# Optimization experiments

Measured on AMD Instinct MI355X. Metric: run time of the kernel, lower is better.

## Reference

```python
import jax, jax.numpy as jnp
import numpy as np

N = 8192
F_IN = 256
F_OUT = 128
SLOPE = 0.2
NEG_INF = -9000000000000000.0


def setup_inputs() -> dict:
    key = jax.random.key(0)
    k1, k2, k3, k4, k5 = jax.random.split(key, 5)
    x = jax.random.normal(k1, (N, F_IN), dtype=jnp.float32)
    adj = jax.random.randint(k2, (N, N), 0, 2).astype(jnp.float32)
    W = jax.random.normal(k3, (F_IN, F_OUT), dtype=jnp.float32) * (1.0 / np.sqrt(F_IN))
    a_src = jax.random.normal(k4, (F_OUT,), dtype=jnp.float32) * (1.0 / np.sqrt(F_OUT))
    a_dst = jax.random.normal(k5, (F_OUT,), dtype=jnp.float32) * (1.0 / np.sqrt(F_OUT))
    return {"x": x, "adj": adj, "W": W, "a_src": a_src, "a_dst": a_dst}


def reference(x, adj, W, a_src, a_dst):
    # h: (N, F_OUT)
    h = x @ W
    f_src = h @ a_src  # (N,)
    f_dst = h @ a_dst  # (N,)
    # additive attention scores: (N, N)
    e = f_src[:, None] + f_dst[None, :]
    e = jnp.where(e >= 0, e, SLOPE * e)  # leaky_relu
    e = jnp.where(adj > 0, e, NEG_INF)
    alpha = jax.nn.softmax(e, axis=1)  # (N, N)
    return alpha @ h  # (N, F_OUT)
```

## Files before the change

### kernel.cpp

```cpp
#include <hip/hip_runtime.h>
#include <hip/hip_bf16.h>

#define NN 8192
#define FIN 256
#define FO 128
#define BROWS 16
#define NCH 32
#define L2E 1.4426950408889634f
#define C2  0.28853900817779268f

typedef __bf16 bf16x8 __attribute__((ext_vector_type(8)));
typedef __bf16 bf16x2 __attribute__((ext_vector_type(2)));
typedef float  f32x4  __attribute__((ext_vector_type(4)));
typedef unsigned long long u64;
typedef u64 u64x2 __attribute__((ext_vector_type(2)));

__device__ __forceinline__ f32x4 ntload(const float* p) {
  return __builtin_nontemporal_load((const f32x4*)p);
}

__global__ __launch_bounds__(256) void k_proj(
    const float* __restrict__ x, const float* __restrict__ W,
    const float* __restrict__ a_src, const float* __restrict__ a_dst,
    __bf16* __restrict__ Bp, float* __restrict__ f_src, float* __restrict__ f_dst)
{
  __shared__ float xs[16 * FIN];
  __shared__ float fs[16], fd[16];
  const int tid = threadIdx.x;
  const int i0 = blockIdx.x * 16;

  const float4* xg = (const float4*)(x + (size_t)i0 * FIN);
  float4* xs4 = (float4*)xs;
  #pragma unroll
  for (int t = 0; t < 4; t++) xs4[tid + 256 * t] = xg[tid + 256 * t];
  if (tid < 16) { fs[tid] = 0.f; fd[tid] = 0.f; }
  __syncthreads();

  const int cq = tid & 31;
  const int rg = tid >> 5;
  const int c0 = cq * 4;
  const int r0 = rg * 2;
  float acc0[4] = {0.f,0.f,0.f,0.f};
  float acc1[4] = {0.f,0.f,0.f,0.f};
  const float* xr0 = xs + r0 * FIN;
  const float* xr1 = xs + (r0 + 1) * FIN;

  for (int k = 0; k < FIN; k += 4) {
    float4 xa = *(const float4*)(xr0 + k);
    float4 xb = *(const float4*)(xr1 + k);
    #pragma unroll
    for (int kk = 0; kk < 4; kk++) {
      float4 wv = *(const float4*)(W + (size_t)(k + kk) * FO + c0);
      float xav = ((const float*)&xa)[kk];
      float xbv = ((const float*)&xb)[kk];
      acc0[0] += xav * wv.x; acc0[1] += xav * wv.y;
      acc0[2] += xav * wv.z; acc0[3] += xav * wv.w;
      acc1[0] += xbv * wv.x; acc1[1] += xbv * wv.y;
      acc1[2] += xbv * wv.z; acc1[3] += xbv * wv.w;
    }
  }

  float4 as = *(const float4*)(a_src + c0);
  float4 ad = *(const float4*)(a_dst + c0);
  float ps0 = acc0[0]*as.x + acc0[1]*as.y + acc0[2]*as.z + acc0[3]*as.w;
  float ps1 = acc1[0]*as.x + acc1[1]*as.y + acc1[2]*as.z + acc1[3]*as.w;
  float pd0 = acc0[0]*ad.x + acc0[1]*ad.y + acc0[2]*ad.z + acc0[3]*ad.w;
  float pd1 = acc1[0]*ad.x + acc1[1]*ad.y + acc1[2]*ad.z + acc1[3]*ad.w;
  atomicAdd(&fs[r0],     ps0);
  atomicAdd(&fs[r0 + 1], ps1);
  atomicAdd(&fd[r0],     pd0);
  atomicAdd(&fd[r0 + 1], pd1);

  const int j0 = i0 + r0;
  const int kg = j0 >> 5;
  const int q  = (j0 >> 3) & 3;
  const int t0 = j0 & 7;
  #pragma unroll
  for (int c = 0; c < 4; c++) {
    const int n = c0 + c;
    bf16x2 v;
    v[0] = (__bf16)acc0[c];
    v[1] = (__bf16)acc1[c];
    size_t idx = ((size_t)(kg * 8 + (n >> 4)) * 64 + q * 16 + (n & 15)) * 8 + t0;
    *(bf16x2*)(Bp + idx) = v;
  }
  __syncthreads();
  if (tid < 16) { f_src[i0 + tid] = fs[tid]; f_dst[i0 + tid] = fd[tid]; }
}

__global__ __launch_bounds__(512, 4) void k_attn(
    const float* __restrict__ adj, const __bf16* __restrict__ Bp,
    const float* __restrict__ f_src, const float* __restrict__ f_dst,
    float* __restrict__ out)
{
  __shared__ __align__(16) float G1s[2][256];
  __shared__ __align__(16) float G2s[2][256];
  __shared__ __align__(16) u64 msk[BROWS][6];
  __shared__ __align__(16) __bf16 af[8][64][8];
  __shared__ float lsum[BROWS];

  const int tid = threadIdx.x;
  const int w = tid >> 6;
  const int lane = tid & 63;
  const int m = lane & 15;
  const int q = lane >> 4;
  const int i0 = blockIdx.x * BROWS;

  const int sqA = w >> 1, kgA = w & 1;
  const int nq8 = w;
  const int tbl = tid >> 8, gcol = tid & 255;

  const float* abase = adj + (size_t)(i0 + 2 * w) * NN + lane * 4;
  f32x4 sA0 = ntload(abase);
  f32x4 sA1 = ntload(abase + NN);
  f32x4 sB0 = ntload(abase + 256);
  f32x4 sB1 = ntload(abase + NN + 256);

  {
    float d0 = f_dst[gcol];
    if (tbl == 0) G1s[0][gcol] = __builtin_amdgcn_exp2f(d0 * L2E);
    else          G2s[0][gcol] = __builtin_amdgcn_exp2f(d0 * C2);
  }
  float fdv = f_dst[256 + gcol];
  if (tid < BROWS) lsum[tid] = 0.f;
  float s = f_src[i0 + m];
  const float F1 = __builtin_amdgcn_exp2f(s * L2E);
  const float F2 = __builtin_amdgcn_exp2f(s * C2);

  f32x4 acc = (f32x4){0.f, 0.f, 0.f, 0.f};
  float psum = 0.f;

#define ITER(c, s0, s1)                                                       \
  {                                                                           \
            \
    u64 b0 = __ballot(s0[0] > 0.f), b1 = __ballot(s0[1] > 0.f);               \
    u64 b2 = __ballot(s0[2] > 0.f), b3 = __ballot(s0[3] > 0.f);               \
    if (lane < 4) msk[2*w][lane]   = lane==0?b0:lane==1?b1:lane==2?b2:b3;     \
    b0 = __ballot(s1[0] > 0.f); b1 = __ballot(s1[1] > 0.f);                   \
    b2 = __ballot(s1[2] > 0.f); b3 = __ballot(s1[3] > 0.f);                   \
    if (lane < 4) msk[2*w+1][lane] = lane==0?b0:lane==1?b1:lane==2?b2:b3;     \
    if ((c) + 1 < NCH) {                                                      \
      if (tbl == 0) G1s[((c)+1)&1][gcol] = __builtin_amdgcn_exp2f(fdv * L2E); \
      else          G2s[((c)+1)&1][gcol] = __builtin_amdgcn_exp2f(fdv * C2);  \
    }                                                                         \
    __syncthreads();                         \
                \
    {                                                                         \
      u64x2 Ma = *(const u64x2*)&msk[m][0];                                   \
      u64x2 Mb = *(const u64x2*)&msk[m][2];                                   \
      const u64 M0 = Ma[0], M1 = Ma[1], M2 = Mb[0], M3 = Mb[1];               \
      const int jl = sqA * 64 + kgA * 32 + q * 8;                             \
      float4 u0 = *(const float4*)(&G1s[(c)&1][jl]);                          \
      float4 u1 = *(const float4*)(&G1s[(c)&1][jl + 4]);                      \
      float4 v0 = *(const float4*)(&G2s[(c)&1][jl]);                          \
      float4 v1 = *(const float4*)(&G2s[(c)&1][jl + 4]);                      \
      const unsigned b = sqA * 16 + kgA * 8 + q * 2;                          \
      const unsigned e0 = (unsigned)(M0 >> b);                                \
      const unsigned e1 = (unsigned)(M1 >> b);                                \
      const unsigned e2 = (unsigned)(M2 >> b);                                \
      const unsigned e3 = (unsigned)(M3 >> b);                                \
      float p0 = (e0 & 1u) ? fmaxf(F1 * u0.x, F2 * v0.x) : 0.f;               \
      float p1 = (e1 & 1u) ? fmaxf(F1 * u0.y, F2 * v0.y) : 0.f;               \
      float p2 = (e2 & 1u) ? fmaxf(F1 * u0.z, F2 * v0.z) : 0.f;               \
      float p3 = (e3 & 1u) ? fmaxf(F1 * u0.w, F2 * v0.w) : 0.f;               \
      float p4 = (e0 & 2u) ? fmaxf(F1 * u1.x, F2 * v1.x) : 0.f;               \
      float p5 = (e1 & 2u) ? fmaxf(F1 * u1.y, F2 * v1.y) : 0.f;               \
      float p6 = (e2 & 2u) ? fmaxf(F1 * u1.z, F2 * v1.z) : 0.f;               \
      float p7 = (e3 & 2u) ? fmaxf(F1 * u1.w, F2 * v1.w) : 0.f;               \
      psum += ((p0 + p1) + (p2 + p3)) + ((p4 + p5) + (p6 + p7));              \
      bf16x8 a;                                                               \
      a[0] = (__bf16)p0; a[1] = (__bf16)p1; a[2] = (__bf16)p2;                \
      a[3] = (__bf16)p3; a[4] = (__bf16)p4; a[5] = (__bf16)p5;                \
      a[6] = (__bf16)p6; a[7] = (__bf16)p7;                                   \
      *(bf16x8*)&af[w][lane][0] = a;                                          \
    }                                                                         \
    __syncthreads();                                   \
                    \
    {                                                                         \
      const __bf16* bch = Bp + (size_t)(c) * 8 * 4096                         \
                          + (size_t)nq8 * 512 + lane * 8;                     \
      bf16x8 bf0 = *(const bf16x8*)(bch);                                     \
      bf16x8 bf1 = *(const bf16x8*)(bch + 4096);                              \
      bf16x8 bf2 = *(const bf16x8*)(bch + 2 * 4096);                          \
      bf16x8 bf3 = *(const bf16x8*)(bch + 3 * 4096);                          \
      bf16x8 bf4 = *(const bf16x8*)(bch + 4 * 4096);                          \
      bf16x8 bf5 = *(const bf16x8*)(bch + 5 * 4096);                          \
      bf16x8 bf6 = *(const bf16x8*)(bch + 6 * 4096);                          \
      bf16x8 bf7 = *(const bf16x8*)(bch + 7 * 4096);                          \
      bf16x8 a0 = *(const bf16x8*)&af[0][lane][0];                            \
      bf16x8 a1 = *(const bf16x8*)&af[1][lane][0];                            \
      bf16x8 a2 = *(const bf16x8*)&af[2][lane][0];                            \
      bf16x8 a3 = *(const bf16x8*)&af[3][lane][0];                            \
      bf16x8 a4 = *(const bf16x8*)&af[4][lane][0];                            \
      bf16x8 a5 = *(const bf16x8*)&af[5][lane][0];                            \
      bf16x8 a6 = *(const bf16x8*)&af[6][lane][0];                            \
      bf16x8 a7 = *(const bf16x8*)&af[7][lane][0];                            \
      acc = __builtin_amdgcn_mfma_f32_16x16x32_bf16(a0, bf0, acc, 0, 0, 0);   \
      acc = __builtin_amdgcn_mfma_f32_16x16x32_bf16(a1, bf1, acc, 0, 0, 0);   \
      acc = __builtin_amdgcn_mfma_f32_16x16x32_bf16(a2, bf2, acc, 0, 0, 0);   \
      acc = __builtin_amdgcn_mfma_f32_16x16x32_bf16(a3, bf3, acc, 0, 0, 0);   \
      acc = __builtin_amdgcn_mfma_f32_16x16x32_bf16(a4, bf4, acc, 0, 0, 0);   \
      acc = __builtin_amdgcn_mfma_f32_16x16x32_bf16(a5, bf5, acc, 0, 0, 0);   \
      acc = __builtin_amdgcn_mfma_f32_16x16x32_bf16(a6, bf6, acc, 0, 0, 0);   \
      acc = __builtin_amdgcn_mfma_f32_16x16x32_bf16(a7, bf7, acc, 0, 0, 0);   \
    }                                                                         \
     \
    if ((c) + 2 < NCH) {                                                      \
      s0 = ntload(abase + ((c) + 2) * 256);                                   \
      s1 = ntload(abase + NN + ((c) + 2) * 256);                              \
      fdv = f_dst[((c) + 2) * 256 + gcol];                                    \
    }                                                                         \
  }

  for (int c = 0; c < NCH; c += 2) {
    ITER(c, sA0, sA1)
    ITER(c + 1, sB0, sB1)
  }
#undef ITER

  {
    float p = psum;
    p += __shfl_xor(p, 16);
    p += __shfl_xor(p, 32);
    if (lane < 16) atomicAdd(&lsum[lane], p);
  }
  __syncthreads();

  #pragma unroll
  for (int r = 0; r < 4; ++r) {
    const int rr = q * 4 + r;
    const float inv = 1.0f / lsum[rr];
    out[(size_t)(i0 + rr) * FO + nq8 * 16 + m] = acc[r] * inv;
  }
}

extern "C" void kernel_launch(void* const* d_in, const int* in_sizes, int n_in,
                              void* d_out, int out_size, void* d_ws, size_t ws_size,
                              hipStream_t stream) {
  const float* x     = (const float*)d_in[0];
  const float* adj   = (const float*)d_in[1];
  const float* W     = (const float*)d_in[2];
  const float* a_src = (const float*)d_in[3];
  const float* a_dst = (const float*)d_in[4];
  float* out = (float*)d_out;

  char* ws = (char*)d_ws;
  __bf16* Bp   = (__bf16*)ws;
  float* f_src = (float*)(ws + 2097152);
  float* f_dst = (float*)(ws + 2097152 + 32768);

  hipLaunchKernelGGL(k_proj, dim3(512), dim3(256), 0, stream,
                     x, W, a_src, a_dst, Bp, f_src, f_dst);
  hipLaunchKernelGGL(k_attn, dim3(512), dim3(512), 0, stream,
                     adj, Bp, f_src, f_dst, out);
}
```

Before: 406.6 us.

## Double the attention chunk width to halve barrier rounds and deepen prefetch

The column chunk processed per iteration grows from 256 to 512, so each step builds masks for twice the columns, fills 16 bf16 A-fragments, and issues 16 MFMAs between barriers. This halves the number of __syncthreads rounds, and each prefetch now keeps eight adj vectors in flight. Scheduling barriers pin the prefetch loads after the MFMA block. In exchange it uses more registers and shared memory, which could reduce occupancy under the 512x4 launch bound.

```diff
diff --git a/kernel.cpp b/kernel.cpp
--- a/kernel.cpp
+++ b/kernel.cpp
@@ -5,7 +5,8 @@
 #define FIN 256
 #define FO 128
 #define BROWS 16
-#define NCH 32
+#define CC 512
+#define NCH 16
 #define L2E 1.4426950408889634f
 #define C2  0.28853900817779268f
 
@@ -93,10 +94,10 @@
     const float* __restrict__ f_src, const float* __restrict__ f_dst,
     float* __restrict__ out)
 {
-  __shared__ __align__(16) float G1s[2][256];
-  __shared__ __align__(16) float G2s[2][256];
-  __shared__ __align__(16) u64 msk[BROWS][6];
-  __shared__ __align__(16) __bf16 af[8][64][8];
+  __shared__ __align__(16) float G1s[2][CC];
+  __shared__ __align__(16) float G2s[2][CC];
+  __shared__ __align__(16) u64 msk[BROWS][10];
+  __shared__ __align__(16) __bf16 af[16][64][8];
   __shared__ float lsum[BROWS];
 
   const int tid = threadIdx.x;
@@ -106,22 +107,33 @@
   const int q = lane >> 4;
   const int i0 = blockIdx.x * BROWS;
 
-  const int sqA = w >> 1, kgA = w & 1;
   const int nq8 = w;
   const int tbl = tid >> 8, gcol = tid & 255;
 
+  float fdvA = f_dst[CC + gcol];
+  float fdvB = f_dst[CC + 256 + gcol];
+  __builtin_amdgcn_sched_barrier(0);
   const float* abase = adj + (size_t)(i0 + 2 * w) * NN + lane * 4;
-  f32x4 sA0 = ntload(abase);
-  f32x4 sA1 = ntload(abase + NN);
-  f32x4 sB0 = ntload(abase + 256);
-  f32x4 sB1 = ntload(abase + NN + 256);
+  f32x4 sA0a = ntload(abase);
+  f32x4 sA0b = ntload(abase + 256);
+  f32x4 sA1a = ntload(abase + NN);
+  f32x4 sA1b = ntload(abase + NN + 256);
+  f32x4 sB0a = ntload(abase + CC);
+  f32x4 sB0b = ntload(abase + CC + 256);
+  f32x4 sB1a = ntload(abase + NN + CC);
+  f32x4 sB1b = ntload(abase + NN + CC + 256);
 
   {
     float d0 = f_dst[gcol];
-    if (tbl == 0) G1s[0][gcol] = __builtin_amdgcn_exp2f(d0 * L2E);
-    else          G2s[0][gcol] = __builtin_amdgcn_exp2f(d0 * C2);
-  }
-  float fdv = f_dst[256 + gcol];
+    float d1 = f_dst[256 + gcol];
+    if (tbl == 0) {
+      G1s[0][gcol]       = __builtin_amdgcn_exp2f(d0 * L2E);
+      G1s[0][256 + gcol] = __builtin_amdgcn_exp2f(d1 * L2E);
+    } else {
+      G2s[0][gcol]       = __builtin_amdgcn_exp2f(d0 * C2);
+      G2s[0][256 + gcol] = __builtin_amdgcn_exp2f(d1 * C2);
+    }
+  }
   if (tid < BROWS) lsum[tid] = 0.f;
   float s = f_src[i0 + m];
   const float F1 = __builtin_amdgcn_exp2f(s * L2E);
@@ -129,32 +141,50 @@
 
   f32x4 acc = (f32x4){0.f, 0.f, 0.f, 0.f};
   float psum = 0.f;
-
-#define ITER(c, s0, s1)                                                       \
+  __syncthreads();
+
+#define ITER(c, s0a, s0b, s1a, s1b)                                           \
   {                                                                           \
-            \
-    u64 b0 = __ballot(s0[0] > 0.f), b1 = __ballot(s0[1] > 0.f);               \
-    u64 b2 = __ballot(s0[2] > 0.f), b3 = __ballot(s0[3] > 0.f);               \
-    if (lane < 4) msk[2*w][lane]   = lane==0?b0:lane==1?b1:lane==2?b2:b3;     \
-    b0 = __ballot(s1[0] > 0.f); b1 = __ballot(s1[1] > 0.f);                   \
-    b2 = __ballot(s1[2] > 0.f); b3 = __ballot(s1[3] > 0.f);                   \
-    if (lane < 4) msk[2*w+1][lane] = lane==0?b0:lane==1?b1:lane==2?b2:b3;     \
+              \
+    {                                                                         \
+      u64 b0 = __ballot(s0a[0] > 0.f), b1 = __ballot(s0a[1] > 0.f);           \
+      u64 b2 = __ballot(s0a[2] > 0.f), b3 = __ballot(s0a[3] > 0.f);           \
+      u64 b4 = __ballot(s0b[0] > 0.f), b5 = __ballot(s0b[1] > 0.f);           \
+      u64 b6 = __ballot(s0b[2] > 0.f), b7 = __ballot(s0b[3] > 0.f);           \
+      if (lane < 8)                                                           \
+        msk[2*w][lane] = lane==0?b0:lane==1?b1:lane==2?b2:lane==3?b3:         \
+                         lane==4?b4:lane==5?b5:lane==6?b6:b7;                 \
+      b0 = __ballot(s1a[0] > 0.f); b1 = __ballot(s1a[1] > 0.f);               \
+      b2 = __ballot(s1a[2] > 0.f); b3 = __ballot(s1a[3] > 0.f);               \
+      b4 = __ballot(s1b[0] > 0.f); b5 = __ballot(s1b[1] > 0.f);               \
+      b6 = __ballot(s1b[2] > 0.f); b7 = __ballot(s1b[3] > 0.f);               \
+      if (lane < 8)                                                           \
+        msk[2*w+1][lane] = lane==0?b0:lane==1?b1:lane==2?b2:lane==3?b3:       \
+                           lane==4?b4:lane==5?b5:lane==6?b6:b7;               \
+    }                                                                         \
     if ((c) + 1 < NCH) {                                                      \
-      if (tbl == 0) G1s[((c)+1)&1][gcol] = __builtin_amdgcn_exp2f(fdv * L2E); \
-      else          G2s[((c)+1)&1][gcol] = __builtin_amdgcn_exp2f(fdv * C2);  \
+      if (tbl == 0) {                                                         \
+        G1s[((c)+1)&1][gcol]       = __builtin_amdgcn_exp2f(fdvA * L2E);      \
+        G1s[((c)+1)&1][256 + gcol] = __builtin_amdgcn_exp2f(fdvB * L2E);      \
+      } else {                                                                \
+        G2s[((c)+1)&1][gcol]       = __builtin_amdgcn_exp2f(fdvA * C2);       \
+        G2s[((c)+1)&1][256 + gcol] = __builtin_amdgcn_exp2f(fdvB * C2);       \
+      }                                                                       \
     }                                                                         \
     __syncthreads();                         \
-                \
-    {                                                                         \
-      u64x2 Ma = *(const u64x2*)&msk[m][0];                                   \
-      u64x2 Mb = *(const u64x2*)&msk[m][2];                                   \
+             \
+    _Pragma("unroll")                                                         \
+    for (int kg = 0; kg < 2; ++kg) {                                          \
+      const int jl = w * 64 + kg * 32 + q * 8;                                \
+      const int g = jl >> 8;                                                  \
+      u64x2 Ma = *(const u64x2*)&msk[m][g * 4];                               \
+      u64x2 Mb = *(const u64x2*)&msk[m][g * 4 + 2];                           \
       const u64 M0 = Ma[0], M1 = Ma[1], M2 = Mb[0], M3 = Mb[1];               \
-      const int jl = sqA * 64 + kgA * 32 + q * 8;                             \
       float4 u0 = *(const float4*)(&G1s[(c)&1][jl]);                          \
       float4 u1 = *(const float4*)(&G1s[(c)&1][jl + 4]);                      \
       float4 v0 = *(const float4*)(&G2s[(c)&1][jl]);                          \
       float4 v1 = *(const float4*)(&G2s[(c)&1][jl + 4]);                      \
-      const unsigned b = sqA * 16 + kgA * 8 + q * 2;                          \
+      const unsigned b = (unsigned)(((w * 16 + kg * 8) & 63) + q * 2);        \
       const unsigned e0 = (unsigned)(M0 >> b);                                \
       const unsigned e1 = (unsigned)(M1 >> b);                                \
       const unsigned e2 = (unsigned)(M2 >> b);                                \
@@ -172,12 +202,13 @@
       a[0] = (__bf16)p0; a[1] = (__bf16)p1; a[2] = (__bf16)p2;                \
       a[3] = (__bf16)p3; a[4] = (__bf16)p4; a[5] = (__bf16)p5;                \
       a[6] = (__bf16)p6; a[7] = (__bf16)p7;                                   \
-      *(bf16x8*)&af[w][lane][0] = a;                                          \
+      *(bf16x8*)&af[w * 2 + kg][lane][0] = a;                                 \
     }                                                                         \
     __syncthreads();                                   \
-                    \
-    {                                                                         \
-      const __bf16* bch = Bp + (size_t)(c) * 8 * 4096                         \
+                \
+    _Pragma("unroll")                                                         \
+    for (int hh = 0; hh < 2; ++hh) {                                          \
+      const __bf16* bch = Bp + (size_t)((c) * 16 + hh * 8) * 4096             \
                           + (size_t)nq8 * 512 + lane * 8;                     \
       bf16x8 bf0 = *(const bf16x8*)(bch);                                     \
       bf16x8 bf1 = *(const bf16x8*)(bch + 4096);                              \
@@ -187,14 +218,14 @@
       bf16x8 bf5 = *(const bf16x8*)(bch + 5 * 4096);                          \
       bf16x8 bf6 = *(const bf16x8*)(bch + 6 * 4096);                          \
       bf16x8 bf7 = *(const bf16x8*)(bch + 7 * 4096);                          \
-      bf16x8 a0 = *(const bf16x8*)&af[0][lane][0];                            \
-      bf16x8 a1 = *(const bf16x8*)&af[1][lane][0];                            \
-      bf16x8 a2 = *(const bf16x8*)&af[2][lane][0];                            \
-      bf16x8 a3 = *(const bf16x8*)&af[3][lane][0];                            \
-      bf16x8 a4 = *(const bf16x8*)&af[4][lane][0];                            \
-      bf16x8 a5 = *(const bf16x8*)&af[5][lane][0];                            \
-      bf16x8 a6 = *(const bf16x8*)&af[6][lane][0];                            \
-      bf16x8 a7 = *(const bf16x8*)&af[7][lane][0];                            \
+      bf16x8 a0 = *(const bf16x8*)&af[hh * 8 + 0][lane][0];                   \
+      bf16x8 a1 = *(const bf16x8*)&af[hh * 8 + 1][lane][0];                   \
+      bf16x8 a2 = *(const bf16x8*)&af[hh * 8 + 2][lane][0];                   \
+      bf16x8 a3 = *(const bf16x8*)&af[hh * 8 + 3][lane][0];                   \
+      bf16x8 a4 = *(const bf16x8*)&af[hh * 8 + 4][lane][0];                   \
+      bf16x8 a5 = *(const bf16x8*)&af[hh * 8 + 5][lane][0];                   \
+      bf16x8 a6 = *(const bf16x8*)&af[hh * 8 + 6][lane][0];                   \
+      bf16x8 a7 = *(const bf16x8*)&af[hh * 8 + 7][lane][0];                   \
       acc = __builtin_amdgcn_mfma_f32_16x16x32_bf16(a0, bf0, acc, 0, 0, 0);   \
       acc = __builtin_amdgcn_mfma_f32_16x16x32_bf16(a1, bf1, acc, 0, 0, 0);   \
       acc = __builtin_amdgcn_mfma_f32_16x16x32_bf16(a2, bf2, acc, 0, 0, 0);   \
@@ -204,17 +235,23 @@
       acc = __builtin_amdgcn_mfma_f32_16x16x32_bf16(a6, bf6, acc, 0, 0, 0);   \
       acc = __builtin_amdgcn_mfma_f32_16x16x32_bf16(a7, bf7, acc, 0, 0, 0);   \
     }                                                                         \
-     \
+              \
+    __builtin_amdgcn_sched_barrier(0);                                        \
     if ((c) + 2 < NCH) {                                                      \
-      s0 = ntload(abase + ((c) + 2) * 256);                                   \
-      s1 = ntload(abase + NN + ((c) + 2) * 256);                              \
-      fdv = f_dst[((c) + 2) * 256 + gcol];                                    \
-    }                                                                         \
+      fdvA = f_dst[((c) + 2) * CC + gcol];                                    \
+      fdvB = f_dst[((c) + 2) * CC + 256 + gcol];                              \
+      const float* nb = abase + ((c) + 2) * CC;                               \
+      s0a = ntload(nb);                                                       \
+      s0b = ntload(nb + 256);                                                 \
+      s1a = ntload(nb + NN);                                                  \
+      s1b = ntload(nb + NN + 256);                                            \
+    }                                                                         \
+    __builtin_amdgcn_sched_barrier(0);                                        \
   }
 
   for (int c = 0; c < NCH; c += 2) {
-    ITER(c, sA0, sA1)
-    ITER(c + 1, sB0, sB1)
+    ITER(c,     sA0a, sA0b, sA1a, sA1b)
+    ITER(c + 1, sB0a, sB0b, sB1a, sB1b)
   }
 #undef ITER
 
```

Result: slower. 432.9 us (+6.5%).
